# Performance work log

Measured on AMD Instinct MI355X. Metric: run time of the kernel, lower is better.

Reference implementation:

```python
import jax, jax.numpy as jnp
import numpy as np

K_NEIGHBORS = 8   # num_neighbors init arg
BETA = 0.5        # smooth-L1 beta
EPS = 1e-8        # torch cosine_similarity eps


def setup_inputs() -> dict:
    key = jax.random.key(0)
    k1, k2, k3 = jax.random.split(key, 3)
    B, N, D, C = 16, 1024, 768, 2
    return {
        "student_emb": jax.random.normal(k1, (B, N, D), dtype=jnp.float32),
        "teacher_emb": jax.random.normal(k2, (B, N, D), dtype=jnp.float32),
        "centers": jax.random.normal(k3, (B, N, C), dtype=jnp.float32),
    }


def _cosine(anchor, nb):
    # anchor [B,N,1,D], nb [B,N,K,D] -> [B,N,K]
    dot = jnp.sum(anchor * nb, axis=-1)
    na = jnp.maximum(jnp.linalg.norm(anchor, axis=-1), EPS)
    nb_n = jnp.maximum(jnp.linalg.norm(nb, axis=-1), EPS)
    return dot / (na * nb_n)


def reference(student_emb, teacher_emb, centers):
    B, N, _ = centers.shape
    k = min(K_NEIGHBORS + 1, N)
    # brute-force pairwise squared distances [B,N,N] (knn_points)
    sq = jnp.sum(centers * centers, axis=-1)
    d2 = sq[:, :, None] + sq[:, None, :] - 2.0 * jnp.einsum("bnc,bmc->bnm", centers, centers)
    _, idx = jax.lax.top_k(-d2, k)   # ascending distance; idx [B,N,k]
    idx = idx[:, :, 1:]               # drop self (distance 0 is first)
    # knn_gather: neighbors [B,N,K,D]
    gather = jax.vmap(lambda e, i: e[i])
    student_nb = gather(student_emb, idx)
    teacher_nb = gather(teacher_emb, idx)
    student_rel = _cosine(student_emb[:, :, None, :], student_nb)  # [B,N,K]
    teacher_rel = jax.lax.stop_gradient(_cosine(teacher_emb[:, :, None, :], teacher_nb))
    diff = jnp.abs(student_rel - teacher_rel)
    sl1 = jnp.where(diff < BETA, 0.5 * diff * diff / BETA, diff - 0.5 * BETA)
    per_patch = sl1.mean(axis=-1)  # [B,N]
    return per_patch.mean()        # reduction='mean'
```

## Files before the change

kernel.cpp:

```cpp
#include <hip/hip_runtime.h>
#include <hip/hip_fp16.h>
#include <math.h>

#define BB 16
#define NN 1024
#define DD 768
#define KK 8
#define BETA_F 0.5f
#define EPS_F 1e-8f

#define TPK_BLOCKS ((BB * NN) / 8)
#define NORM_BLOCKS ((BB * NN) / 4)

typedef _Float16 h2_t __attribute__((ext_vector_type(2)));

#if defined(__has_builtin)
#if __has_builtin(__builtin_amdgcn_fdot2)
#define HAVE_FDOT2 1
#endif
#endif

__device__ __forceinline__ float dot4acc(uint2 a, uint2 b, float acc) {
#ifdef HAVE_FDOT2
    acc = __builtin_amdgcn_fdot2(__builtin_bit_cast(h2_t, a.x),
                                 __builtin_bit_cast(h2_t, b.x), acc, false);
    acc = __builtin_amdgcn_fdot2(__builtin_bit_cast(h2_t, a.y),
                                 __builtin_bit_cast(h2_t, b.y), acc, false);
#else
    float2 fa = __half22float2(__builtin_bit_cast(__half2, a.x));
    float2 fb = __half22float2(__builtin_bit_cast(__half2, b.x));
    acc = fmaf(fa.x, fb.x, acc); acc = fmaf(fa.y, fb.y, acc);
    fa = __half22float2(__builtin_bit_cast(__half2, a.y));
    fb = __half22float2(__builtin_bit_cast(__half2, b.y));
    acc = fmaf(fa.x, fb.x, acc); acc = fmaf(fa.y, fb.y, acc);
#endif
    return acc;
}

__device__ __forceinline__ unsigned wave_min_u32_to_all(unsigned x) {
    int v = (int)x;
#define STEP(CTRL, RM) {                                                    \
        int y_ = __builtin_amdgcn_update_dpp(v, v, CTRL, RM, 0xf, false);   \
        v = (int)((unsigned)v < (unsigned)y_ ? (unsigned)v : (unsigned)y_); \
    }
    STEP(0x111, 0xf)
    STEP(0x112, 0xf)
    STEP(0x114, 0xf)
    STEP(0x118, 0xf)
    STEP(0x142, 0xa)
    STEP(0x143, 0xc)
#undef STEP
    return (unsigned)__builtin_amdgcn_readlane(v, 63);
}

__device__ __forceinline__ unsigned topk_u(float anx, float any_, float sqn, float4 c) {
    float dot = anx * c.x + any_ * c.y;
    float d2  = (sqn + c.z) - 2.0f * dot;
    unsigned int u = __float_as_uint(d2);
    u ^= (unsigned int)((int)u >> 31) | 0x80000000u;
    return u;
}

struct KeysU { unsigned k[16]; };

__device__ __forceinline__ void initkeysu(KeysU& K, float anx, float any_, float sqn,
                                          const float4* c4, int lane) {
#pragma unroll
    for (int i = 0; i < 16; ++i) {
        const int m_ = i * 64 + lane;
        K.k[i] = topk_u(anx, any_, sqn, c4[m_]);
    }
}

__device__ __forceinline__ unsigned umin2(unsigned a, unsigned b) { return a < b ? a : b; }

__device__ __forceinline__ unsigned mintreeu(const KeysU& K) {
    return umin2(umin2(umin2(umin2(K.k[0], K.k[1]),  umin2(K.k[2], K.k[3])),
                       umin2(umin2(K.k[4], K.k[5]),  umin2(K.k[6], K.k[7]))),
                 umin2(umin2(umin2(K.k[8], K.k[9]),  umin2(K.k[10], K.k[11])),
                       umin2(umin2(K.k[12], K.k[13]), umin2(K.k[14], K.k[15]))));
}

__device__ __forceinline__ void topk_wave_body(const float* __restrict__ centers,
                                               int* __restrict__ idx_out,
                                               int tb, int tid, float4* c4) {
    const int b    = tb >> 7;
    const int grp  = tb & 127;
    const int wave = tid >> 6;
    const int lane = tid & 63;

    const float4* cbase = (const float4*)(centers + (size_t)b * NN * 2);
    for (int i = tid; i < NN / 2; i += 256) {
        float4 v = cbase[i];
        c4[2 * i + 0] = make_float4(v.x, v.y, v.x * v.x + v.y * v.y, 0.f);
        c4[2 * i + 1] = make_float4(v.z, v.w, v.z * v.z + v.w * v.w, 0.f);
    }
    __syncthreads();

    const int nA = grp * 8 + wave * 2;
    const int nB = nA + 1;
    const float4 cA = c4[nA];
    const float4 cB = c4[nB];

    KeysU KA, KB;
    initkeysu(KA, cA.x, cA.y, cA.z, c4, lane);
    initkeysu(KB, cB.x, cB.y, cB.z, c4, lane);

    unsigned lmA = mintreeu(KA);
    unsigned lmB = mintreeu(KB);

    int* rowA = idx_out + ((size_t)b * NN + nA) * KK;
    int* rowB = rowA + KK;

#pragma unroll 1
    for (int r = 0; r < 9; ++r) {
        const unsigned gA = wave_min_u32_to_all(lmA);
        const unsigned gB = wave_min_u32_to_all(lmB);

        unsigned mA = 0xffffffffu, mB = 0xffffffffu;
#pragma unroll
        for (int i = 15; i >= 0; --i) {
            unsigned long long bA = __ballot(KA.k[i] == gA);
            unsigned long long bB = __ballot(KB.k[i] == gB);
            mA = bA ? (unsigned)(i * 64) + (unsigned)__builtin_ctzll(bA) : mA;
            mB = bB ? (unsigned)(i * 64) + (unsigned)__builtin_ctzll(bB) : mB;
        }

        if (r > 0 && lane == 0) {
            rowA[r - 1] = (int)mA;
            rowB[r - 1] = (int)mB;
        }

        const unsigned iwA = mA >> 6, lwA = mA & 63;
        const unsigned iwB = mB >> 6, lwB = mB & 63;
        const bool winA = ((unsigned)lane == lwA);
        const bool winB = ((unsigned)lane == lwB);
#pragma unroll
        for (int i = 0; i < 16; ++i) {
            KA.k[i] = ((unsigned)i == iwA && winA) ? 0xffffffffu : KA.k[i];
            KB.k[i] = ((unsigned)i == iwB && winB) ? 0xffffffffu : KB.k[i];
        }
        lmA = mintreeu(KA);
        lmB = mintreeu(KB);
    }
}

__global__ __launch_bounds__(256) void topk_kernel(const float* __restrict__ centers,
                                                   int* __restrict__ idx_out) {
    __shared__ float4 c4[NN];
    topk_wave_body(centers, idx_out, blockIdx.x, threadIdx.x, c4);
}

__global__ __launch_bounds__(256) void normh_kernel(const float* __restrict__ s,
                                                    const float* __restrict__ t,
                                                    __half* __restrict__ ns,
                                                    __half* __restrict__ nt) {
    const int row  = blockIdx.x * 4 + (threadIdx.x >> 6);
    const int lane = threadIdx.x & 63;
    const float4* srow = (const float4*)(s + (size_t)row * DD);
    const float4* trow = (const float4*)(t + (size_t)row * DD);
    float4 vs[3], vt[3];
    float ss = 0.f, tt = 0.f;
#pragma unroll
    for (int i = 0; i < 3; ++i) {
        vs[i] = srow[lane + 64 * i];
        vt[i] = trow[lane + 64 * i];
        ss = fmaf(vs[i].x, vs[i].x, fmaf(vs[i].y, vs[i].y,
             fmaf(vs[i].z, vs[i].z, fmaf(vs[i].w, vs[i].w, ss))));
        tt = fmaf(vt[i].x, vt[i].x, fmaf(vt[i].y, vt[i].y,
             fmaf(vt[i].z, vt[i].z, fmaf(vt[i].w, vt[i].w, tt))));
    }
#pragma unroll
    for (int m = 1; m < 64; m <<= 1) {
        ss += __shfl_xor(ss, m);
        tt += __shfl_xor(tt, m);
    }
    const float is_ = 1.0f / fmaxf(sqrtf(ss), EPS_F);
    const float it_ = 1.0f / fmaxf(sqrtf(tt), EPS_F);

    uint2* nsrow = (uint2*)(ns + (size_t)row * DD);
    uint2* ntrow = (uint2*)(nt + (size_t)row * DD);
#pragma unroll
    for (int i = 0; i < 3; ++i) {
        __half2 a0 = __floats2half2_rn(vs[i].x * is_, vs[i].y * is_);
        __half2 a1 = __floats2half2_rn(vs[i].z * is_, vs[i].w * is_);
        __half2 b0 = __floats2half2_rn(vt[i].x * it_, vt[i].y * it_);
        __half2 b1 = __floats2half2_rn(vt[i].z * it_, vt[i].w * it_);
        uint2 ua; ua.x = __builtin_bit_cast(unsigned int, a0);
        ua.y = __builtin_bit_cast(unsigned int, a1);
        uint2 ub; ub.x = __builtin_bit_cast(unsigned int, b0);
        ub.y = __builtin_bit_cast(unsigned int, b1);
        nsrow[lane + 64 * i] = ua;
        ntrow[lane + 64 * i] = ub;
    }
}

__global__ __launch_bounds__(256) void lossh_kernel(const __half* __restrict__ ns,
                                                    const __half* __restrict__ nt,
                                                    const int* __restrict__ idx,
                                                    float* __restrict__ part) {
    const int bid  = blockIdx.x;
    const int v    = (bid & 7) * 512 + (bid >> 3);
    const int wave = threadIdx.x >> 6;
    const int lane = threadIdx.x & 63;
    const int p    = v * 4 + wave;
    const int base = p & ~(NN - 1);

    int q[8];
    {
        const int4* ip = (const int4*)(idx + (size_t)p * KK);
        int4 a = ip[0], c = ip[1];
        q[0] = base + a.x; q[1] = base + a.y; q[2] = base + a.z; q[3] = base + a.w;
        q[4] = base + c.x; q[5] = base + c.y; q[6] = base + c.z; q[7] = base + c.w;
    }

    const uint2* srow = (const uint2*)(ns + (size_t)p * DD);
    const uint2* trow = (const uint2*)(nt + (size_t)p * DD);
    uint2 sa[3], ta[3];
#pragma unroll
    for (int c = 0; c < 3; ++c) {
        sa[c] = srow[lane + 64 * c];
        ta[c] = trow[lane + 64 * c];
    }

    uint2 sv[8][3], tv[8][3];
#pragma unroll
    for (int j = 0; j < 8; ++j) {
        const uint2* snb = (const uint2*)(ns + (size_t)q[j] * DD);
        const uint2* tnb = (const uint2*)(nt + (size_t)q[j] * DD);
#pragma unroll
        for (int c = 0; c < 3; ++c) {
            sv[j][c] = snb[lane + 64 * c];
            tv[j][c] = tnb[lane + 64 * c];
        }
    }

    float ds[8], dt[8];
#pragma unroll
    for (int j = 0; j < 8; ++j) {
        float a = 0.f, b = 0.f;
#pragma unroll
        for (int c = 0; c < 3; ++c) {
            a = dot4acc(sa[c], sv[j][c], a);
            b = dot4acc(ta[c], tv[j][c], b);
        }
        ds[j] = a;
        dt[j] = b;
    }
#pragma unroll
    for (int m = 1; m < 64; m <<= 1) {
#pragma unroll
        for (int j = 0; j < 8; ++j) {
            ds[j] += __shfl_xor(ds[j], m);
            dt[j] += __shfl_xor(dt[j], m);
        }
    }
    float sum = 0.f;
#pragma unroll
    for (int j = 0; j < 8; ++j) {
        const float diff = fabsf(ds[j] - dt[j]);
        sum += diff < BETA_F ? (0.5f * diff * diff / BETA_F) : (diff - 0.5f * BETA_F);
    }

    __shared__ float wpart[4];
    if (lane == 0) wpart[wave] = sum;
    __syncthreads();
    if (threadIdx.x == 0)
        part[v] = (wpart[0] + wpart[1]) + (wpart[2] + wpart[3]);
}

__global__ __launch_bounds__(256) void norm_kernel(const float* __restrict__ s,
                                                   const float* __restrict__ t,
                                                   float* __restrict__ inv_s,
                                                   float* __restrict__ inv_t) {
    const int row  = blockIdx.x * 4 + (threadIdx.x >> 6);
    const int lane = threadIdx.x & 63;
    const float4* srow = (const float4*)(s + (size_t)row * DD);
    const float4* trow = (const float4*)(t + (size_t)row * DD);
    float ss = 0.f, tt = 0.f;
#pragma unroll
    for (int i = 0; i < 3; ++i) {
        float4 v = srow[lane + 64 * i];
        ss = fmaf(v.x, v.x, fmaf(v.y, v.y, fmaf(v.z, v.z, fmaf(v.w, v.w, ss))));
        float4 w = trow[lane + 64 * i];
        tt = fmaf(w.x, w.x, fmaf(w.y, w.y, fmaf(w.z, w.z, fmaf(w.w, w.w, tt))));
    }
#pragma unroll
    for (int m = 1; m < 64; m <<= 1) {
        ss += __shfl_xor(ss, m);
        tt += __shfl_xor(tt, m);
    }
    if (lane == 0) {
        inv_s[row] = 1.0f / fmaxf(sqrtf(ss), EPS_F);
        inv_t[row] = 1.0f / fmaxf(sqrtf(tt), EPS_F);
    }
}

__global__ __launch_bounds__(256) void lossf_kernel(const float* __restrict__ s,
                                                    const float* __restrict__ t,
                                                    const int* __restrict__ idx,
                                                    const float* __restrict__ inv_s,
                                                    const float* __restrict__ inv_t,
                                                    float* __restrict__ part) {
    const int wave = threadIdx.x >> 6;
    const int lane = threadIdx.x & 63;
    const int p    = blockIdx.x * 4 + wave;
    const int base = p & ~(NN - 1);
    int q[8];
    {
        const int4* ip = (const int4*)(idx + (size_t)p * KK);
        int4 a = ip[0], c = ip[1];
        q[0] = base + a.x; q[1] = base + a.y; q[2] = base + a.z; q[3] = base + a.w;
        q[4] = base + c.x; q[5] = base + c.y; q[6] = base + c.z; q[7] = base + c.w;
    }
    float isq[8], itq[8];
#pragma unroll
    for (int j = 0; j < 8; ++j) { isq[j] = inv_s[q[j]]; itq[j] = inv_t[q[j]]; }
    const float isn = inv_s[p];
    const float itn = inv_t[p];
    const float4* srow = (const float4*)(s + (size_t)p * DD);
    const float4* trow = (const float4*)(t + (size_t)p * DD);
    float4 as0 = srow[lane], as1 = srow[lane + 64], as2 = srow[lane + 128];
    float4 at0 = trow[lane], at1 = trow[lane + 64], at2 = trow[lane + 128];
    float ds[8], dt[8];
#pragma unroll
    for (int j = 0; j < 8; ++j) {
        const float4* snb = (const float4*)(s + (size_t)q[j] * DD);
        const float4* tnb = (const float4*)(t + (size_t)q[j] * DD);
        float4 v0 = snb[lane], v1 = snb[lane + 64], v2 = snb[lane + 128];
        float4 w0 = tnb[lane], w1 = tnb[lane + 64], w2 = tnb[lane + 128];
        float a = 0.f, b = 0.f;
        a = fmaf(as0.x, v0.x, a); a = fmaf(as0.y, v0.y, a);
        a = fmaf(as0.z, v0.z, a); a = fmaf(as0.w, v0.w, a);
        a = fmaf(as1.x, v1.x, a); a = fmaf(as1.y, v1.y, a);
        a = fmaf(as1.z, v1.z, a); a = fmaf(as1.w, v1.w, a);
        a = fmaf(as2.x, v2.x, a); a = fmaf(as2.y, v2.y, a);
        a = fmaf(as2.z, v2.z, a); a = fmaf(as2.w, v2.w, a);
        b = fmaf(at0.x, w0.x, b); b = fmaf(at0.y, w0.y, b);
        b = fmaf(at0.z, w0.z, b); b = fmaf(at0.w, w0.w, b);
        b = fmaf(at1.x, w1.x, b); b = fmaf(at1.y, w1.y, b);
        b = fmaf(at1.z, w1.z, b); b = fmaf(at1.w, w1.w, b);
        b = fmaf(at2.x, w2.x, b); b = fmaf(at2.y, w2.y, b);
        b = fmaf(at2.z, w2.z, b); b = fmaf(at2.w, w2.w, b);
        ds[j] = a; dt[j] = b;
    }
#pragma unroll
    for (int m = 1; m < 64; m <<= 1) {
#pragma unroll
        for (int j = 0; j < 8; ++j) {
            ds[j] += __shfl_xor(ds[j], m);
            dt[j] += __shfl_xor(dt[j], m);
        }
    }
    float sum = 0.f;
#pragma unroll
    for (int j = 0; j < 8; ++j) {
        const float cs   = ds[j] * isn * isq[j];
        const float ct   = dt[j] * itn * itq[j];
        const float diff = fabsf(cs - ct);
        sum += diff < BETA_F ? (0.5f * diff * diff / BETA_F) : (diff - 0.5f * BETA_F);
    }
    __shared__ float wpart[4];
    if (lane == 0) wpart[wave] = sum;
    __syncthreads();
    if (threadIdx.x == 0)
        part[blockIdx.x] = (wpart[0] + wpart[1]) + (wpart[2] + wpart[3]);
}

__global__ __launch_bounds__(256) void finalize_kernel(const float* __restrict__ part,
                                                       float* __restrict__ out) {
    __shared__ float red[256];
    float acc = 0.f;
    for (int i = threadIdx.x; i < (BB * NN) / 4; i += 256) acc += part[i];
    red[threadIdx.x] = acc;
    __syncthreads();
    for (int off = 128; off > 0; off >>= 1) {
        if (threadIdx.x < off) red[threadIdx.x] += red[threadIdx.x + off];
        __syncthreads();
    }
    if (threadIdx.x == 0) out[0] = red[0] * (1.0f / (float)(BB * NN * KK));
}

extern "C" void kernel_launch(void* const* d_in, const int* in_sizes, int n_in,
                              void* d_out, int out_size, void* d_ws, size_t ws_size,
                              hipStream_t stream) {
    const float* student = (const float*)d_in[0];
    const float* teacher = (const float*)d_in[1];
    const float* centers = (const float*)d_in[2];
    float* out = (float*)d_out;

    const size_t idx_bytes  = (size_t)BB * NN * KK * sizeof(int);
    const size_t half_bytes = (size_t)BB * NN * DD * sizeof(__half);
    const size_t part_bytes = 4096 * sizeof(float);
    int* idx_buf = (int*)d_ws;

    if (ws_size >= idx_bytes + 2 * half_bytes + part_bytes) {
        __half* ns  = (__half*)((char*)d_ws + idx_bytes);
        __half* nt  = ns + (size_t)BB * NN * DD;
        float* part = (float*)((char*)d_ws + idx_bytes + 2 * half_bytes);
        topk_kernel<<<TPK_BLOCKS, 256, 0, stream>>>(centers, idx_buf);
        normh_kernel<<<NORM_BLOCKS, 256, 0, stream>>>(student, teacher, ns, nt);
        lossh_kernel<<<NORM_BLOCKS, 256, 0, stream>>>(ns, nt, idx_buf, part);
        finalize_kernel<<<1, 256, 0, stream>>>(part, out);
    } else {
        float* inv_s = (float*)((char*)d_ws + idx_bytes);
        float* inv_t = inv_s + BB * NN;
        float* part  = inv_t + BB * NN;
        topk_kernel<<<TPK_BLOCKS, 256, 0, stream>>>(centers, idx_buf);
        norm_kernel<<<NORM_BLOCKS, 256, 0, stream>>>(student, teacher, inv_s, inv_t);
        lossf_kernel<<<NORM_BLOCKS, 256, 0, stream>>>(student, teacher, idx_buf,
                                                      inv_s, inv_t, part);
        finalize_kernel<<<1, 256, 0, stream>>>(part, out);
    }
}
```

Baseline: 98.52 us.

## Fuse top-k and normalization kernels into one interleaved launch, simplify argmin locate

```diff
diff --git a/kernel.cpp b/kernel.cpp
--- a/kernel.cpp
+++ b/kernel.cpp
@@ -10,7 +10,8 @@
 #define EPS_F 1e-8f
 
 #define TPK_BLOCKS ((BB * NN) / 8)
-#define NORM_BLOCKS ((BB * NN) / 4)
+#define NORM2_BLOCKS ((BB * NN) / 8)
+#define LOSS_BLOCKS ((BB * NN) / 4)
 
 typedef _Float16 h2_t __attribute__((ext_vector_type(2)));
 
@@ -81,13 +82,27 @@
                        umin2(umin2(K.k[12], K.k[13]), umin2(K.k[14], K.k[15]))));
 }
 
+__device__ __forceinline__ unsigned locate_m(const KeysU& K, unsigned g, unsigned lane) {
+    unsigned mloc = 0xffffffffu;
+#pragma unroll
+    for (int i = 0; i < 16; ++i)
+        mloc = umin2(mloc, K.k[i] == g ? (unsigned)(i * 64) + lane : 0xffffffffu);
+    return mloc;
+}
+
+__device__ __forceinline__ void kill_m(KeysU& K, unsigned mg, unsigned lane) {
+#pragma unroll
+    for (int i = 0; i < 16; ++i)
+        K.k[i] = ((unsigned)(i * 64) + lane == mg) ? 0xffffffffu : K.k[i];
+}
+
 __device__ __forceinline__ void topk_wave_body(const float* __restrict__ centers,
                                                int* __restrict__ idx_out,
                                                int tb, int tid, float4* c4) {
     const int b    = tb >> 7;
     const int grp  = tb & 127;
     const int wave = tid >> 6;
-    const int lane = tid & 63;
+    const unsigned lane = tid & 63;
 
     const float4* cbase = (const float4*)(centers + (size_t)b * NN * 2);
     for (int i = tid; i < NN / 2; i += 256) {
@@ -117,29 +132,16 @@
         const unsigned gA = wave_min_u32_to_all(lmA);
         const unsigned gB = wave_min_u32_to_all(lmB);
 
-        unsigned mA = 0xffffffffu, mB = 0xffffffffu;
-#pragma unroll
-        for (int i = 15; i >= 0; --i) {
-            unsigned long long bA = __ballot(KA.k[i] == gA);
-            unsigned long long bB = __ballot(KB.k[i] == gB);
-            mA = bA ? (unsigned)(i * 64) + (unsigned)__builtin_ctzll(bA) : mA;
-            mB = bB ? (unsigned)(i * 64) + (unsigned)__builtin_ctzll(bB) : mB;
+        const unsigned mgA = wave_min_u32_to_all(locate_m(KA, gA, lane));
+        const unsigned mgB = wave_min_u32_to_all(locate_m(KB, gB, lane));
+
+        if (r > 0 && lane == 0) {
+            rowA[r - 1] = (int)mgA;
+            rowB[r - 1] = (int)mgB;
         }
 
-        if (r > 0 && lane == 0) {
-            rowA[r - 1] = (int)mA;
-            rowB[r - 1] = (int)mB;
-        }
-
-        const unsigned iwA = mA >> 6, lwA = mA & 63;
-        const unsigned iwB = mB >> 6, lwB = mB & 63;
-        const bool winA = ((unsigned)lane == lwA);
-        const bool winB = ((unsigned)lane == lwB);
-#pragma unroll
-        for (int i = 0; i < 16; ++i) {
-            KA.k[i] = ((unsigned)i == iwA && winA) ? 0xffffffffu : KA.k[i];
-            KB.k[i] = ((unsigned)i == iwB && winB) ? 0xffffffffu : KB.k[i];
-        }
+        kill_m(KA, mgA, lane);
+        kill_m(KB, mgB, lane);
         lmA = mintreeu(KA);
         lmB = mintreeu(KB);
     }
@@ -151,48 +153,89 @@
     topk_wave_body(centers, idx_out, blockIdx.x, threadIdx.x, c4);
 }
 
-__global__ __launch_bounds__(256) void normh_kernel(const float* __restrict__ s,
-                                                    const float* __restrict__ t,
-                                                    __half* __restrict__ ns,
-                                                    __half* __restrict__ nt) {
-    const int row  = blockIdx.x * 4 + (threadIdx.x >> 6);
-    const int lane = threadIdx.x & 63;
-    const float4* srow = (const float4*)(s + (size_t)row * DD);
-    const float4* trow = (const float4*)(t + (size_t)row * DD);
-    float4 vs[3], vt[3];
-    float ss = 0.f, tt = 0.f;
+__device__ __forceinline__ void normh2_body(const float* __restrict__ s,
+                                            const float* __restrict__ t,
+                                            __half* __restrict__ ns,
+                                            __half* __restrict__ nt,
+                                            int nb, int tid) {
+    const int wave = tid >> 6;
+    const int lane = tid & 63;
+    const int row0 = nb * 8 + wave * 2;
+    const int row1 = row0 + 1;
+    const float4* s0 = (const float4*)(s + (size_t)row0 * DD);
+    const float4* t0 = (const float4*)(t + (size_t)row0 * DD);
+    const float4* s1 = (const float4*)(s + (size_t)row1 * DD);
+    const float4* t1 = (const float4*)(t + (size_t)row1 * DD);
+
+    float4 vs0[3], vt0[3], vs1[3], vt1[3];
 #pragma unroll
     for (int i = 0; i < 3; ++i) {
-        vs[i] = srow[lane + 64 * i];
-        vt[i] = trow[lane + 64 * i];
-        ss = fmaf(vs[i].x, vs[i].x, fmaf(vs[i].y, vs[i].y,
-             fmaf(vs[i].z, vs[i].z, fmaf(vs[i].w, vs[i].w, ss))));
-        tt = fmaf(vt[i].x, vt[i].x, fmaf(vt[i].y, vt[i].y,
-             fmaf(vt[i].z, vt[i].z, fmaf(vt[i].w, vt[i].w, tt))));
+        vs0[i] = s0[lane + 64 * i];
+        vt0[i] = t0[lane + 64 * i];
+        vs1[i] = s1[lane + 64 * i];
+        vt1[i] = t1[lane + 64 * i];
+    }
+    float ss0 = 0.f, tt0 = 0.f, ss1 = 0.f, tt1 = 0.f;
+#pragma unroll
+    for (int i = 0; i < 3; ++i) {
+        ss0 = fmaf(vs0[i].x, vs0[i].x, fmaf(vs0[i].y, vs0[i].y,
+              fmaf(vs0[i].z, vs0[i].z, fmaf(vs0[i].w, vs0[i].w, ss0))));
+        tt0 = fmaf(vt0[i].x, vt0[i].x, fmaf(vt0[i].y, vt0[i].y,
+              fmaf(vt0[i].z, vt0[i].z, fmaf(vt0[i].w, vt0[i].w, tt0))));
+        ss1 = fmaf(vs1[i].x, vs1[i].x, fmaf(vs1[i].y, vs1[i].y,
+              fmaf(vs1[i].z, vs1[i].z, fmaf(vs1[i].w, vs1[i].w, ss1))));
+        tt1 = fmaf(vt1[i].x, vt1[i].x, fmaf(vt1[i].y, vt1[i].y,
+              fmaf(vt1[i].z, vt1[i].z, fmaf(vt1[i].w, vt1[i].w, tt1))));
     }
 #pragma unroll
     for (int m = 1; m < 64; m <<= 1) {
-        ss += __shfl_xor(ss, m);
-        tt += __shfl_xor(tt, m);
-    }
-    const float is_ = 1.0f / fmaxf(sqrtf(ss), EPS_F);
-    const float it_ = 1.0f / fmaxf(sqrtf(tt), EPS_F);
-
-    uint2* nsrow = (uint2*)(ns + (size_t)row * DD);
-    uint2* ntrow = (uint2*)(nt + (size_t)row * DD);
+        ss0 += __shfl_xor(ss0, m);
+        tt0 += __shfl_xor(tt0, m);
+        ss1 += __shfl_xor(ss1, m);
+        tt1 += __shfl_xor(tt1, m);
+    }
+    const float is0 = 1.0f / fmaxf(sqrtf(ss0), EPS_F);
+    const float it0 = 1.0f / fmaxf(sqrtf(tt0), EPS_F);
+    const float is1 = 1.0f / fmaxf(sqrtf(ss1), EPS_F);
+    const float it1 = 1.0f / fmaxf(sqrtf(tt1), EPS_F);
+
+    uint2* ns0 = (uint2*)(ns + (size_t)row0 * DD);
+    uint2* nt0 = (uint2*)(nt + (size_t)row0 * DD);
+    uint2* ns1 = (uint2*)(ns + (size_t)row1 * DD);
+    uint2* nt1 = (uint2*)(nt + (size_t)row1 * DD);
 #pragma unroll
     for (int i = 0; i < 3; ++i) {
-        __half2 a0 = __floats2half2_rn(vs[i].x * is_, vs[i].y * is_);
-        __half2 a1 = __floats2half2_rn(vs[i].z * is_, vs[i].w * is_);
-        __half2 b0 = __floats2half2_rn(vt[i].x * it_, vt[i].y * it_);
-        __half2 b1 = __floats2half2_rn(vt[i].z * it_, vt[i].w * it_);
-        uint2 ua; ua.x = __builtin_bit_cast(unsigned int, a0);
-        ua.y = __builtin_bit_cast(unsigned int, a1);
-        uint2 ub; ub.x = __builtin_bit_cast(unsigned int, b0);
-        ub.y = __builtin_bit_cast(unsigned int, b1);
-        nsrow[lane + 64 * i] = ua;
-        ntrow[lane + 64 * i] = ub;
-    }
+        __half2 a0 = __floats2half2_rn(vs0[i].x * is0, vs0[i].y * is0);
+        __half2 a1 = __floats2half2_rn(vs0[i].z * is0, vs0[i].w * is0);
+        __half2 b0 = __floats2half2_rn(vt0[i].x * it0, vt0[i].y * it0);
+        __half2 b1 = __floats2half2_rn(vt0[i].z * it0, vt0[i].w * it0);
+        __half2 c0 = __floats2half2_rn(vs1[i].x * is1, vs1[i].y * is1);
+        __half2 c1 = __floats2half2_rn(vs1[i].z * is1, vs1[i].w * is1);
+        __half2 d0 = __floats2half2_rn(vt1[i].x * it1, vt1[i].y * it1);
+        __half2 d1 = __floats2half2_rn(vt1[i].z * it1, vt1[i].w * it1);
+        uint2 ua, ub, uc, ud;
+        ua.x = __builtin_bit_cast(unsigned int, a0); ua.y = __builtin_bit_cast(unsigned int, a1);
+        ub.x = __builtin_bit_cast(unsigned int, b0); ub.y = __builtin_bit_cast(unsigned int, b1);
+        uc.x = __builtin_bit_cast(unsigned int, c0); uc.y = __builtin_bit_cast(unsigned int, c1);
+        ud.x = __builtin_bit_cast(unsigned int, d0); ud.y = __builtin_bit_cast(unsigned int, d1);
+        ns0[lane + 64 * i] = ua;
+        nt0[lane + 64 * i] = ub;
+        ns1[lane + 64 * i] = uc;
+        nt1[lane + 64 * i] = ud;
+    }
+}
+
+__global__ __launch_bounds__(256) void fused_prep(const float* __restrict__ centers,
+                                                  const float* __restrict__ s,
+                                                  const float* __restrict__ t,
+                                                  int* __restrict__ idx_out,
+                                                  __half* __restrict__ ns,
+                                                  __half* __restrict__ nt) {
+    __shared__ float4 c4[NN];
+    if (blockIdx.x & 1)
+        normh2_body(s, t, ns, nt, blockIdx.x >> 1, threadIdx.x);
+    else
+        topk_wave_body(centers, idx_out, blockIdx.x >> 1, threadIdx.x, c4);
 }
 
 __global__ __launch_bounds__(256) void lossh_kernel(const __half* __restrict__ ns,
@@ -398,17 +441,17 @@
         __half* ns  = (__half*)((char*)d_ws + idx_bytes);
         __half* nt  = ns + (size_t)BB * NN * DD;
         float* part = (float*)((char*)d_ws + idx_bytes + 2 * half_bytes);
-        topk_kernel<<<TPK_BLOCKS, 256, 0, stream>>>(centers, idx_buf);
-        normh_kernel<<<NORM_BLOCKS, 256, 0, stream>>>(student, teacher, ns, nt);
-        lossh_kernel<<<NORM_BLOCKS, 256, 0, stream>>>(ns, nt, idx_buf, part);
+        fused_prep<<<TPK_BLOCKS + NORM2_BLOCKS, 256, 0, stream>>>(centers, student,
+                                                                  teacher, idx_buf, ns, nt);
+        lossh_kernel<<<LOSS_BLOCKS, 256, 0, stream>>>(ns, nt, idx_buf, part);
         finalize_kernel<<<1, 256, 0, stream>>>(part, out);
     } else {
         float* inv_s = (float*)((char*)d_ws + idx_bytes);
         float* inv_t = inv_s + BB * NN;
         float* part  = inv_t + BB * NN;
         topk_kernel<<<TPK_BLOCKS, 256, 0, stream>>>(centers, idx_buf);
-        norm_kernel<<<NORM_BLOCKS, 256, 0, stream>>>(student, teacher, inv_s, inv_t);
-        lossf_kernel<<<NORM_BLOCKS, 256, 0, stream>>>(student, teacher, idx_buf,
+        norm_kernel<<<LOSS_BLOCKS, 256, 0, stream>>>(student, teacher, inv_s, inv_t);
+        lossf_kernel<<<LOSS_BLOCKS, 256, 0, stream>>>(student, teacher, idx_buf,
                                                       inv_s, inv_t, part);
         finalize_kernel<<<1, 256, 0, stream>>>(part, out);
     }
```

New measurement: 99.11 us. About the same (+0.6%).
